# Kernel tuning notes

Hardware: AMD Instinct MI355X
Metric: run time of the kernel (lower is better)

The kernel has to match this reference:

```python
import jax, jax.numpy as jnp
import numpy as np

B, N, F_IN, OUT_FEATS, NUM_CLS, NUM_INDS = 256, 200, 200, 256, 8, 512
PCT_EDGES = 20
K = int(PCT_EDGES / 100 * N * (N - 1) / 2)  # 3980 hard edges
TAU = 1.0


def setup_inputs() -> dict:
    key = jax.random.key(0)
    ks = jax.random.split(key, 6)
    x = jax.random.normal(ks[0], (B, N, F_IN), dtype=jnp.float32)
    gumbel_u = jax.random.uniform(ks[1], (B, N, N), dtype=jnp.float32)
    nets = jax.random.normal(ks[2], (NUM_INDS, N, N), dtype=jnp.float32)
    w_gnn = jax.random.normal(ks[3], (F_IN, OUT_FEATS), dtype=jnp.float32) / np.sqrt(F_IN).astype(np.float32)
    w_lin = jax.random.normal(ks[4], (OUT_FEATS, NUM_CLS), dtype=jnp.float32) / np.sqrt(OUT_FEATS).astype(np.float32)
    b_lin = jnp.zeros((NUM_CLS,), dtype=jnp.float32)
    net_index = jax.random.randint(ks[5], (B,), 0, NUM_INDS)
    return {"x": x, "gumbel_u": gumbel_u, "nets": nets, "w_gnn": w_gnn,
            "w_lin": w_lin, "b_lin": b_lin, "net_index": net_index}


def _gumbel_softkmax(logits, u, k, tau):
    # logits: [B, N, N]; u: uniform(0,1) noise -> Gumbel(0,1) via -log(-log(u))
    b, n, _ = logits.shape
    g = -jnp.log(-jnp.log(jnp.clip(u, 1e-10, 1.0 - 1e-10)))
    g = (logits + g) / tau
    sym = (g + jnp.swapaxes(g, 1, 2)) * 0.5                      # symmetrize
    y_soft = jax.nn.softmax(sym.reshape(b, -1), axis=-1).reshape(b, n, n)
    upper_flat = jnp.triu(y_soft).reshape(b, -1)                 # upper tri incl. diag
    _, idx = jax.lax.top_k(upper_flat, k)                        # [B, k]
    y_hard = jnp.zeros_like(upper_flat).at[jnp.arange(b)[:, None], idx].set(1.0)
    y_hard = y_hard.reshape(b, n, n)
    diag = jnp.diagonal(y_hard, axis1=-2, axis2=-1)              # [B, N]
    eye = jnp.eye(n, dtype=y_hard.dtype)
    y_hard = y_hard + jnp.swapaxes(y_hard, 1, 2) - diag[:, :, None] * eye
    # straight-through estimator
    return y_hard - jax.lax.stop_gradient(y_soft) + y_soft


def reference(x, gumbel_u, nets, w_gnn, w_lin, b_lin, net_index):
    selected = nets[net_index]                                   # [B, N, N]
    adj = _gumbel_softkmax(selected, gumbel_u, K, TAU)
    # gnn: relu(adj @ x @ W_gnn)  -> embeddings [B, N, OUT_FEATS]
    emb = jax.nn.relu(jnp.einsum('bij,bjf,fo->bio', adj, x, w_gnn))
    out = emb @ w_lin + b_lin                                    # [B, N, NUM_CLS]
    return out, emb, adj
```

## Files before the change

kernel.cpp:

```cpp
#include <hip/hip_runtime.h>
#include <math.h>

#define B_SZ 256
#define N_SZ 200
#define NN (N_SZ * N_SZ)
#define FIN 200
#define OUT_F 256
#define NCLS 8
#define KSEL 3980
#define NUPPER 20100
#define KSTRIDE 20128
#define NT 7
#define NTILES 28

#define ADJ_STRIDE 224
#define KGRP_PB 25
#define XWM_PB (KGRP_PB * 2048)

#define EMB_OFF (B_SZ * N_SZ * NCLS)
#define ADJ_OFF (EMB_OFF + B_SZ * N_SZ * OUT_F)

#define KEYS_OFF_B   0
#define WKG_OFF_B    26214400
#define ADJB16_OFF_B 26329088

typedef unsigned short ushort_t;
typedef float f32x4 __attribute__((ext_vector_type(4)));
typedef short bf16x8 __attribute__((ext_vector_type(8)));
typedef ushort_t u16x4 __attribute__((ext_vector_type(4)));
typedef ushort_t u16x8 __attribute__((ext_vector_type(8)));

__device__ __forceinline__ unsigned sortkey(float f) {
    unsigned u = __float_as_uint(f);
    return (u & 0x80000000u) ? ~u : (u | 0x80000000u);
}

__device__ __forceinline__ ushort_t f2b(float f) {
    unsigned u = __float_as_uint(f);
    return (ushort_t)((u + 0x7FFFu + ((u >> 16) & 1u)) >> 16);
}

__device__ __forceinline__ bf16x8 f2b8(float4 lo, float4 hi) {
    bf16x8 r;
    r[0] = (short)f2b(lo.x); r[1] = (short)f2b(lo.y);
    r[2] = (short)f2b(lo.z); r[3] = (short)f2b(lo.w);
    r[4] = (short)f2b(hi.x); r[5] = (short)f2b(hi.y);
    r[6] = (short)f2b(hi.z); r[7] = (short)f2b(hi.w);
    return r;
}

__device__ __forceinline__ void tile_decode(int t, int& ti, int& tj) {
    int a = 0, rem = t;
    while (rem >= NT - a) { rem -= NT - a; ++a; }
    ti = a; tj = a + rem;
}

__global__ __launch_bounds__(256) void kA(
    const float* __restrict__ gu, const float* __restrict__ nets,
    const int* __restrict__ net_index, unsigned* __restrict__ keys,
    const float* __restrict__ wg, ushort_t* __restrict__ wkg)
{
    const int blk = blockIdx.x;
    if (blk >= B_SZ * NTILES) {
        int pb = blk - B_SZ * NTILES;
        int e = pb * 256 + threadIdx.x;
        int kg = e >> 11;
        int rem = e & 2047;
        int n = rem >> 3;
        int ki = rem & 7;
        int k = kg * 8 + ki;
        wkg[e] = (k < FIN) ? f2b(wg[k * OUT_F + n]) : (ushort_t)0;
        return;
    }
    const int b = blk / NTILES;
    int ti, tj; tile_decode(blk % NTILES, ti, tj);
    const int i0 = ti * 32, j0 = tj * 32;
    const float* ub = gu + (size_t)b * NN;
    const float* lb = nets + (size_t)net_index[b] * NN;

    __shared__ float Hij[32][33];
    __shared__ float Hji[32][33];

    const int r = threadIdx.x >> 5;
    const int c = threadIdx.x & 31;

    #pragma unroll
    for (int s = 0; s < 4; ++s) {
        int rr = r + 8 * s;
        int i = i0 + rr, j = j0 + c;
        if (i < N_SZ && j < N_SZ) {
            float u = ub[i * N_SZ + j];
            u = fminf(fmaxf(u, 1e-10f), 1.0f - 1e-10f);
            Hij[rr][c] = lb[i * N_SZ + j] - logf(-logf(u));
        }
        if (ti != tj) {
            int i2 = j0 + rr, j2 = i0 + c;
            if (i2 < N_SZ && j2 < N_SZ) {
                float u = ub[i2 * N_SZ + j2];
                u = fminf(fmaxf(u, 1e-10f), 1.0f - 1e-10f);
                Hji[rr][c] = lb[i2 * N_SZ + j2] - logf(-logf(u));
            }
        }
    }
    __syncthreads();

    unsigned* kb = keys + (size_t)b * KSTRIDE;
    #pragma unroll
    for (int s = 0; s < 4; ++s) {
        int rr = r + 8 * s;
        int i = i0 + rr, j = j0 + c;
        if (i < N_SZ && j < N_SZ && i <= j) {
            float hji = (ti == tj) ? Hij[c][rr] : Hji[c][rr];
            float sv = 0.5f * (Hij[rr][c] + hji);
            int base = i * N_SZ - (i * (i - 1)) / 2;
            kb[base + (j - i)] = sortkey(sv);
        }
    }
}

__global__ __launch_bounds__(512) void kSelW(
    const unsigned* __restrict__ keys, float* __restrict__ out_base,
    ushort_t* __restrict__ adjb16)
{
    const int b = blockIdx.x;
    const int tid = threadIdx.x;
    __shared__ __align__(16) unsigned kl[NUPPER];
    __shared__ unsigned hist[256];
    __shared__ unsigned sfx[256];
    __shared__ unsigned scanA[512];
    __shared__ unsigned sPrefix;
    __shared__ int sKK;

    {
        const int4* kb4 = (const int4*)(keys + (size_t)b * KSTRIDE);
        int4* kl4 = (int4*)kl;
        for (int q = tid; q < 5025; q += 512) kl4[q] = kb4[q];
    }

    unsigned prefix = 0;
    int kk = KSEL;
    for (int round = 0; round < 4; ++round) {
        const int shift = 24 - 8 * round;
        if (tid < 256) hist[tid] = 0;
        __syncthreads();
        for (int idx = tid; idx < NUPPER; idx += 512) {
            unsigned key = kl[idx];
            bool in = (round == 0) || ((key >> (shift + 8)) == prefix);
            if (in) atomicAdd(&hist[(key >> shift) & 255u], 1u);
        }
        __syncthreads();
        if (tid < 256) sfx[tid] = hist[tid];
        __syncthreads();
        #pragma unroll
        for (int off = 1; off < 256; off <<= 1) {
            unsigned add = 0;
            if (tid < 256 && tid + off < 256) add = sfx[tid + off];
            __syncthreads();
            if (tid < 256) sfx[tid] += add;
            __syncthreads();
        }
        if (tid < 256) {
            unsigned above = (tid < 255) ? sfx[tid + 1] : 0u;
            if (sfx[tid] >= (unsigned)kk && above < (unsigned)kk) {
                sPrefix = (prefix << 8) | (unsigned)tid;
                sKK = kk - (int)above;
            }
        }
        __syncthreads();
        prefix = sPrefix;
        kk = sKK;
        __syncthreads();
    }
    const unsigned kth = prefix;

    const int lo = tid * 40;
    const int hi = (lo + 40 < NUPPER) ? lo + 40 : NUPPER;
    unsigned mycnt = 0;
    for (int idx = lo; idx < hi; ++idx)
        if (kl[idx] == kth) ++mycnt;
    scanA[tid] = mycnt;
    __syncthreads();
    #pragma unroll
    for (int off = 1; off < 512; off <<= 1) {
        unsigned add = (tid >= off) ? scanA[tid - off] : 0u;
        __syncthreads();
        scanA[tid] += add;
        __syncthreads();
    }
    unsigned rank = scanA[tid] - mycnt;
    for (int idx = lo; idx < hi; ++idx) {
        unsigned key = kl[idx];
        unsigned dec;
        if (key > kth) dec = 1u;
        else if (key == kth) { dec = (rank < (unsigned)kk) ? 1u : 0u; ++rank; }
        else dec = 0u;
        kl[idx] = dec;
    }
    __syncthreads();

    float* adj = out_base + ADJ_OFF + (size_t)b * NN;
    for (int e = tid; e < 10000; e += 512) {
        int i = e / 50;
        int j0 = (e % 50) * 4;
        int bi = i * N_SZ - (i * (i - 1)) / 2 - i;
        float4 v;
        float* vp = (float*)&v;
        #pragma unroll
        for (int q = 0; q < 4; ++q) {
            int j = j0 + q;
            int pk = (i <= j) ? (bi + j)
                              : (j * N_SZ - (j * (j - 1)) / 2 + (i - j));
            vp[q] = kl[pk] ? 1.0f : 0.0f;
        }
        *(float4*)(adj + (size_t)i * N_SZ + j0) = v;
    }
    ushort_t* ab = adjb16 + (size_t)b * (N_SZ * ADJ_STRIDE);
    for (int e = tid; e < 5600; e += 512) {
        int i = e / 28;
        int j0 = (e % 28) * 8;
        int bi = i * N_SZ - (i * (i - 1)) / 2 - i;
        u16x8 v;
        #pragma unroll
        for (int q = 0; q < 8; ++q) {
            int j = j0 + q;
            ushort_t o = 0;
            if (j < N_SZ) {
                int pk = (i <= j) ? (bi + j)
                                  : (j * N_SZ - (j * (j - 1)) / 2 + (i - j));
                o = kl[pk] ? (ushort_t)0x3F80 : (ushort_t)0;
            }
            v[q] = o;
        }
        *(u16x8*)(ab + (size_t)i * ADJ_STRIDE + j0) = v;
    }
}

__global__ __launch_bounds__(256) void k2_mfma(
    const float* __restrict__ x, const ushort_t* __restrict__ wkg,
    ushort_t* __restrict__ xwm)
{
    const int r0 = blockIdx.x * 64;
    const int tid = threadIdx.x;
    const int w = tid >> 6;
    const int l = tid & 63;
    const int g = l >> 4;
    const int r = l & 15;

    __shared__ __align__(16) ushort_t Cs[64 * 256];

    f32x4 acc[4][4];
    #pragma unroll
    for (int mf = 0; mf < 4; ++mf)
        #pragma unroll
        for (int nf = 0; nf < 4; ++nf)
            acc[mf][nf] = (f32x4){0.f, 0.f, 0.f, 0.f};

    for (int c = 0; c < 7; ++c) {
        const int koff = (c * 32 + g * 8 < FIN) ? (c * 32 + g * 8) : 0;
        bf16x8 af[4], bf[4];
        #pragma unroll
        for (int mf = 0; mf < 4; ++mf) {
            const float* ap = x + (size_t)(r0 + mf * 16 + r) * FIN + koff;
            float4 lo = *(const float4*)ap;
            float4 hi = *(const float4*)(ap + 4);
            af[mf] = f2b8(lo, hi);
        }
        #pragma unroll
        for (int nf = 0; nf < 4; ++nf)
            bf[nf] = *(const bf16x8*)(wkg + c * 8192 + g * 2048 + (w * 64 + nf * 16 + r) * 8);
        #pragma unroll
        for (int mf = 0; mf < 4; ++mf)
            #pragma unroll
            for (int nf = 0; nf < 4; ++nf)
                acc[mf][nf] = __builtin_amdgcn_mfma_f32_16x16x32_bf16(
                    af[mf], bf[nf], acc[mf][nf], 0, 0, 0);
    }

    #pragma unroll
    for (int mf = 0; mf < 4; ++mf) {
        #pragma unroll
        for (int jj = 0; jj < 4; ++jj) {
            int row = mf * 16 + g * 4 + jj;
            #pragma unroll
            for (int nf = 0; nf < 4; ++nf) {
                int col = w * 64 + nf * 16 + r;
                Cs[((row >> 3) << 11) + col * 8 + (row & 7)] = f2b(acc[mf][nf][jj]);
            }
        }
    }
    __syncthreads();
    #pragma unroll
    for (int kg = 0; kg < 8; ++kg) {
        int grow0 = r0 + kg * 8;
        int bb = grow0 / N_SZ;
        int jb = grow0 % N_SZ;
        ushort_t* dst = xwm + (size_t)bb * XWM_PB + ((jb >> 3) << 11);
        *(int4*)(dst + tid * 8) = *(const int4*)(Cs + (kg << 11) + tid * 8);
    }
}

__global__ __launch_bounds__(256) void k3_fused(
    const ushort_t* __restrict__ adjb16, const ushort_t* __restrict__ xwm,
    const float* __restrict__ wl, const float* __restrict__ bl,
    float* __restrict__ out_base)
{
    const int blk = blockIdx.x;
    const int xcd = blk & 7;
    const int idx = blk >> 3;
    const int b = xcd + 8 * (idx / 13);
    const int mt = idx % 13;
    const int tid = threadIdx.x;
    const int w = tid >> 6;
    const int l = tid & 63;
    const int g = l >> 4;
    const int r = l & 15;

    const ushort_t* adjb = adjb16 + (size_t)b * (N_SZ * ADJ_STRIDE);
    const ushort_t* xwb = xwm + (size_t)b * XWM_PB;

    __shared__ __align__(16) float Es[16 * 256];
    float (*red)[4][4][8] = (float(*)[4][4][8])Es;

    int arow = mt * 16 + r; if (arow > N_SZ - 1) arow = N_SZ - 1;
    bf16x8 aa[7];
    #pragma unroll
    for (int c = 0; c < 7; ++c)
        aa[c] = *(const bf16x8*)(adjb + arow * ADJ_STRIDE + c * 32 + g * 8);

    f32x4 acc[4];
    #pragma unroll
    for (int nf = 0; nf < 4; ++nf) acc[nf] = (f32x4){0.f, 0.f, 0.f, 0.f};

    #pragma unroll
    for (int c = 0; c < 7; ++c) {
        bf16x8 bf[4];
        #pragma unroll
        for (int nf = 0; nf < 4; ++nf)
            bf[nf] = *(const bf16x8*)(xwb + c * 8192 + g * 2048 + (w * 64 + nf * 16 + r) * 8);
        #pragma unroll
        for (int nf = 0; nf < 4; ++nf)
            acc[nf] = __builtin_amdgcn_mfma_f32_16x16x32_bf16(
                aa[c], bf[nf], acc[nf], 0, 0, 0);
    }

    #pragma unroll
    for (int j = 0; j < 4; ++j) {
        int rowl = g * 4 + j;
        #pragma unroll
        for (int nf = 0; nf < 4; ++nf)
            Es[rowl * 256 + w * 64 + nf * 16 + r] = fmaxf(acc[nf][j], 0.0f);
    }
    __syncthreads();
    #pragma unroll
    for (int q = 0; q < 4; ++q) {
        int e = q * 256 + tid;
        int rowl = e >> 6;
        int c4 = e & 63;
        int grow = mt * 16 + rowl;
        if (grow < N_SZ) {
            float4 v = *(const float4*)(Es + rowl * 256 + c4 * 4);
            *(float4*)(out_base + EMB_OFF + ((size_t)b * N_SZ + grow) * OUT_F + c4 * 4) = v;
        }
    }
    __syncthreads();

    float wlv[4][NCLS];
    #pragma unroll
    for (int nf = 0; nf < 4; ++nf) {
        int col = w * 64 + nf * 16 + r;
        #pragma unroll
        for (int cls = 0; cls < NCLS; ++cls) wlv[nf][cls] = wl[col * NCLS + cls];
    }
    #pragma unroll
    for (int j = 0; j < 4; ++j) {
        float e0 = fmaxf(acc[0][j], 0.0f);
        float e1 = fmaxf(acc[1][j], 0.0f);
        float e2 = fmaxf(acc[2][j], 0.0f);
        float e3 = fmaxf(acc[3][j], 0.0f);
        float pr[NCLS];
        #pragma unroll
        for (int cls = 0; cls < NCLS; ++cls)
            pr[cls] = e0 * wlv[0][cls] + e1 * wlv[1][cls]
                    + e2 * wlv[2][cls] + e3 * wlv[3][cls];
        #pragma unroll
        for (int off = 1; off <= 8; off <<= 1) {
            #pragma unroll
            for (int cls = 0; cls < NCLS; ++cls)
                pr[cls] += __shfl_xor(pr[cls], off, 64);
        }
        if (r < NCLS) red[w][g][j][r] = pr[r];
    }
    __syncthreads();

    if (tid < 16 * NCLS) {
        int rowl = tid >> 3, cls = tid & 7;
        int gg = rowl >> 2, jj = rowl & 3;
        int grow = mt * 16 + rowl;
        if (grow < N_SZ) {
            float s = red[0][gg][jj][cls] + red[1][gg][jj][cls]
                    + red[2][gg][jj][cls] + red[3][gg][jj][cls] + bl[cls];
            out_base[((size_t)b * N_SZ + grow) * NCLS + cls] = s;
        }
    }
}

extern "C" void kernel_launch(void* const* d_in, const int* in_sizes, int n_in,
                              void* d_out, int out_size, void* d_ws, size_t ws_size,
                              hipStream_t stream) {
    const float* x    = (const float*)d_in[0];
    const float* gu   = (const float*)d_in[1];
    const float* nets = (const float*)d_in[2];
    const float* wg   = (const float*)d_in[3];
    const float* wl   = (const float*)d_in[4];
    const float* bl   = (const float*)d_in[5];
    const int*   nidx = (const int*)d_in[6];
    float* out = (float*)d_out;

    char* ws = (char*)d_ws;
    unsigned* keys    = (unsigned*)(ws + KEYS_OFF_B);
    ushort_t* xwm     = (ushort_t*)(ws + KEYS_OFF_B);
    ushort_t* wkg     = (ushort_t*)(ws + WKG_OFF_B);
    ushort_t* adjb16  = (ushort_t*)(ws + ADJB16_OFF_B);

    kA<<<B_SZ * NTILES + 224, 256, 0, stream>>>(gu, nets, nidx, keys, wg, wkg);
    kSelW<<<B_SZ, 512, 0, stream>>>(keys, out, adjb16);
    k2_mfma<<<(B_SZ * N_SZ) / 64, 256, 0, stream>>>(x, wkg, xwm);
    k3_fused<<<B_SZ * 13, 256, 0, stream>>>(adjb16, xwm, wl, bl, out);
}
```

Before: 149.5 us.

## Use per-row bitmask for selected edges and double kSelW block size

The selection kernel now runs 1024 threads per batch block instead of 512, so each thread handles 20 upper-triangle keys rather than 40. Instead of overwriting the key array with 0/1 decisions and then re-deriving triangular indices for every output element, each selected edge sets bits in a shared N×7 bitmask for both (i,j) and (j,i) using atomicOr. The fp32 and bf16 adjacency writers then read one mask word per vector and expand its bits. This removes the scattered triangular-index reads from shared memory in the output phase, at the cost of shared-memory atomics, a per-thread binary search for the starting row, and a longer scan.

Result: faster. 139.1 us (-6.9%).

```diff
diff --git a/kernel.cpp b/kernel.cpp
--- a/kernel.cpp
+++ b/kernel.cpp
@@ -53,6 +53,10 @@
     int a = 0, rem = t;
     while (rem >= NT - a) { rem -= NT - a; ++a; }
     ti = a; tj = a + rem;
+}
+
+__device__ __forceinline__ int rowbase(int i) {
+    return i * N_SZ - (i * (i - 1)) / 2;
 }
 
 __global__ __launch_bounds__(256) void kA(
@@ -111,14 +115,14 @@
         int i = i0 + rr, j = j0 + c;
         if (i < N_SZ && j < N_SZ && i <= j) {
             float hji = (ti == tj) ? Hij[c][rr] : Hji[c][rr];
-            float sv = 0.5f * (Hij[rr][c] + hji);
+            float sv = 0.5f * ((Hij[rr][c]) + hji);
             int base = i * N_SZ - (i * (i - 1)) / 2;
             kb[base + (j - i)] = sortkey(sv);
         }
     }
 }
 
-__global__ __launch_bounds__(512) void kSelW(
+__global__ __launch_bounds__(1024) void kSelW(
     const unsigned* __restrict__ keys, float* __restrict__ out_base,
     ushort_t* __restrict__ adjb16)
 {
@@ -127,15 +131,17 @@
     __shared__ __align__(16) unsigned kl[NUPPER];
     __shared__ unsigned hist[256];
     __shared__ unsigned sfx[256];
-    __shared__ unsigned scanA[512];
+    __shared__ unsigned scanA[1024];
+    __shared__ unsigned M[N_SZ][7];
     __shared__ unsigned sPrefix;
     __shared__ int sKK;
 
     {
         const int4* kb4 = (const int4*)(keys + (size_t)b * KSTRIDE);
         int4* kl4 = (int4*)kl;
-        for (int q = tid; q < 5025; q += 512) kl4[q] = kb4[q];
-    }
+        for (int q = tid; q < 5025; q += 1024) kl4[q] = kb4[q];
+    }
+    for (int q = tid; q < N_SZ * 7; q += 1024) ((unsigned*)M)[q] = 0;
 
     unsigned prefix = 0;
     int kk = KSEL;
@@ -143,7 +149,7 @@
         const int shift = 24 - 8 * round;
         if (tid < 256) hist[tid] = 0;
         __syncthreads();
-        for (int idx = tid; idx < NUPPER; idx += 512) {
+        for (int idx = tid; idx < NUPPER; idx += 1024) {
             unsigned key = kl[idx];
             bool in = (round == 0) || ((key >> (shift + 8)) == prefix);
             if (in) atomicAdd(&hist[(key >> shift) & 255u], 1u);
@@ -173,63 +179,68 @@
     }
     const unsigned kth = prefix;
 
-    const int lo = tid * 40;
-    const int hi = (lo + 40 < NUPPER) ? lo + 40 : NUPPER;
+    const int lo = tid * 20;
+    const int hi = (lo + 20 < NUPPER) ? lo + 20 : NUPPER;
     unsigned mycnt = 0;
     for (int idx = lo; idx < hi; ++idx)
         if (kl[idx] == kth) ++mycnt;
     scanA[tid] = mycnt;
     __syncthreads();
     #pragma unroll
-    for (int off = 1; off < 512; off <<= 1) {
+    for (int off = 1; off < 1024; off <<= 1) {
         unsigned add = (tid >= off) ? scanA[tid - off] : 0u;
         __syncthreads();
         scanA[tid] += add;
         __syncthreads();
     }
     unsigned rank = scanA[tid] - mycnt;
-    for (int idx = lo; idx < hi; ++idx) {
-        unsigned key = kl[idx];
-        unsigned dec;
-        if (key > kth) dec = 1u;
-        else if (key == kth) { dec = (rank < (unsigned)kk) ? 1u : 0u; ++rank; }
-        else dec = 0u;
-        kl[idx] = dec;
+
+    if (lo < NUPPER) {
+        int iLo = 0, iHi = N_SZ - 1;
+        while (iLo < iHi) {
+            int mid = (iLo + iHi + 1) >> 1;
+            if (rowbase(mid) <= lo) iLo = mid; else iHi = mid - 1;
+        }
+        int i = iLo;
+        int nextBase = rowbase(i + 1);
+        for (int idx = lo; idx < hi; ++idx) {
+            while (idx >= nextBase) { ++i; nextBase = rowbase(i + 1); }
+            unsigned key = kl[idx];
+            bool dec;
+            if (key > kth) dec = true;
+            else if (key == kth) { dec = (rank < (unsigned)kk); ++rank; }
+            else dec = false;
+            if (dec) {
+                int j = i + (idx - rowbase(i));
+                atomicOr(&M[i][j >> 5], 1u << (j & 31));
+                atomicOr(&M[j][i >> 5], 1u << (i & 31));
+            }
+        }
     }
     __syncthreads();
 
     float* adj = out_base + ADJ_OFF + (size_t)b * NN;
-    for (int e = tid; e < 10000; e += 512) {
+    for (int e = tid; e < 10000; e += 1024) {
         int i = e / 50;
         int j0 = (e % 50) * 4;
-        int bi = i * N_SZ - (i * (i - 1)) / 2 - i;
+        unsigned wbits = M[i][j0 >> 5] >> (j0 & 31);
         float4 v;
-        float* vp = (float*)&v;
-        #pragma unroll
-        for (int q = 0; q < 4; ++q) {
-            int j = j0 + q;
-            int pk = (i <= j) ? (bi + j)
-                              : (j * N_SZ - (j * (j - 1)) / 2 + (i - j));
-            vp[q] = kl[pk] ? 1.0f : 0.0f;
-        }
+        v.x = (wbits & 1u) ? 1.0f : 0.0f;
+        v.y = (wbits & 2u) ? 1.0f : 0.0f;
+        v.z = (wbits & 4u) ? 1.0f : 0.0f;
+        v.w = (wbits & 8u) ? 1.0f : 0.0f;
         *(float4*)(adj + (size_t)i * N_SZ + j0) = v;
     }
     ushort_t* ab = adjb16 + (size_t)b * (N_SZ * ADJ_STRIDE);
-    for (int e = tid; e < 5600; e += 512) {
+    for (int e = tid; e < 5600; e += 1024) {
         int i = e / 28;
         int j0 = (e % 28) * 8;
-        int bi = i * N_SZ - (i * (i - 1)) / 2 - i;
+        unsigned wbits = (j0 < N_SZ) ? (M[i][j0 >> 5] >> (j0 & 31)) : 0u;
         u16x8 v;
         #pragma unroll
         for (int q = 0; q < 8; ++q) {
             int j = j0 + q;
-            ushort_t o = 0;
-            if (j < N_SZ) {
-                int pk = (i <= j) ? (bi + j)
-                                  : (j * N_SZ - (j * (j - 1)) / 2 + (i - j));
-                o = kl[pk] ? (ushort_t)0x3F80 : (ushort_t)0;
-            }
-            v[q] = o;
+            v[q] = (j < N_SZ && (wbits & (1u << q))) ? (ushort_t)0x3F80 : (ushort_t)0;
         }
         *(u16x8*)(ab + (size_t)i * ADJ_STRIDE + j0) = v;
     }
@@ -423,7 +434,7 @@
     ushort_t* adjb16  = (ushort_t*)(ws + ADJB16_OFF_B);
 
     kA<<<B_SZ * NTILES + 224, 256, 0, stream>>>(gu, nets, nidx, keys, wg, wkg);
-    kSelW<<<B_SZ, 512, 0, stream>>>(keys, out, adjb16);
+    kSelW<<<B_SZ, 1024, 0, stream>>>(keys, out, adjb16);
     k2_mfma<<<(B_SZ * N_SZ) / 64, 256, 0, stream>>>(x, wkg, xwm);
     k3_fused<<<B_SZ * 13, 256, 0, stream>>>(adjb16, xwm, wl, bl, out);
 }
```
